# Performance work log

Measured on AMD Instinct MI355X. Metric: run time of the kernel, lower is better.

## Reference

```python
import jax, jax.numpy as jnp
import numpy as np

T, B, H = 1024, 16, 1024
S = 2048


def setup_inputs() -> dict:
    key = jax.random.key(0)
    k1, k2, k3, k4 = jax.random.split(key, 4)
    output = jax.random.normal(k1, (T, B, H), dtype=jnp.float32)
    memory = jax.random.normal(k2, (S, B, H), dtype=jnp.float32)
    attn_mask = jnp.zeros((B, T, S), dtype=jnp.bool_)  # True = masked
    # linear_out: Linear(2H -> H); torch weight layout [out, in]
    W = jax.random.normal(k3, (H, 2 * H), dtype=jnp.float32) * (1.0 / np.sqrt(2 * H))
    b = jax.random.normal(k4, (H,), dtype=jnp.float32) * 0.01
    return {"output": output, "memory": memory, "attn_mask": attn_mask, "W": W, "b": b}


def reference(output, memory, attn_mask, W, b):
    # scores: (B, T, S) = output^T @ memory (unscaled dot product)
    attn = jnp.einsum('tbh,sbh->bts', output, memory)
    attn = jnp.where(attn_mask, -jnp.inf, attn)
    attn = jax.nn.softmax(attn, axis=2)
    # context: (T, B, H)
    context = jnp.einsum('bts,sbh->tbh', attn, memory)
    combined = jnp.concatenate([context, output], axis=2)  # (T, B, 2H)
    out = jnp.tanh(jnp.einsum('tbd,hd->tbh', combined, W) + b)
    return (out, attn)
```

## Files before the change

kernel.cpp:

```cpp
#include <hip/hip_runtime.h>
#include <hip/hip_bf16.h>
#include <math.h>

#define Tn 1024
#define Bn 16
#define Hn 1024
#define Sn 2048

typedef __attribute__((ext_vector_type(8))) short bf16x8;
typedef __attribute__((ext_vector_type(8))) unsigned short u16x8;
typedef __attribute__((ext_vector_type(4))) float f32x4;

__device__ __forceinline__ unsigned short f2bf(float x) {
  unsigned u = __float_as_uint(x);
  u += 0x7fffu + ((u >> 16) & 1u);
  return (unsigned short)(u >> 16);
}
__device__ __forceinline__ float bf2f(unsigned short h) {
  return __uint_as_float(((unsigned)h) << 16);
}

__device__ __forceinline__ void gload16(const void* g, void* l) {
  __builtin_amdgcn_global_load_lds((const __attribute__((address_space(1))) void*)g,
                                   (__attribute__((address_space(3))) void*)l, 16, 0, 0);
}

__device__ __forceinline__ int xcd_swz(int bid, int nwg) {
  return (bid & 7) * (nwg >> 3) + (bid >> 3);
}

__device__ __forceinline__ f32x4 mfma16(bf16x8 a, bf16x8 b, f32x4 c) {
  return __builtin_amdgcn_mfma_f32_16x16x32_bf16(a, b, c, 0, 0, 0);
}


__global__ __launch_bounds__(256) void k_split_plane(const float* __restrict__ src,
                                                     unsigned short* __restrict__ hiP,
                                                     unsigned short* __restrict__ loP,
                                                     int rows) {
  const int i = blockIdx.x * 256 + threadIdx.x;
  const int h8 = i & (Hn / 8 - 1);
  const int rem = i >> 7;
  const int b = rem & (Bn - 1);
  const int r = rem >> 4;
  const float4 a = *(const float4*)(src + (size_t)i * 8);
  const float4 c = *(const float4*)(src + (size_t)i * 8 + 4);
  const float v[8] = {a.x, a.y, a.z, a.w, c.x, c.y, c.z, c.w};
  u16x8 hv, lv;
#pragma unroll
  for (int j = 0; j < 8; ++j) {
    const unsigned short h = f2bf(v[j]);
    hv[j] = h;
    lv[j] = f2bf(v[j] - bf2f(h));
  }
  const size_t dst = ((size_t)b * rows + r) * Hn + h8 * 8;
  *(u16x8*)(hiP + dst) = hv;
  *(u16x8*)(loP + dst) = lv;
}

__global__ __launch_bounds__(256) void k_cvt8(const float* __restrict__ src,
                                              unsigned short* __restrict__ dst, int n8) {
  const int i = blockIdx.x * 256 + threadIdx.x;
  if (i >= n8) return;
  const float4 a = *(const float4*)(src + (size_t)i * 8);
  const float4 c = *(const float4*)(src + (size_t)i * 8 + 4);
  u16x8 u;
  u[0] = f2bf(a.x); u[1] = f2bf(a.y); u[2] = f2bf(a.z); u[3] = f2bf(a.w);
  u[4] = f2bf(c.x); u[5] = f2bf(c.y); u[6] = f2bf(c.z); u[7] = f2bf(c.w);
  *(u16x8*)(dst + (size_t)i * 8) = u;
}

__global__ __launch_bounds__(256) void k_trH(const unsigned short* __restrict__ memH,
                                             unsigned short* __restrict__ memT) {
  __shared__ unsigned short L[64 * 72];
  const int t = threadIdx.x;
  const int h0 = blockIdx.x * 64, s0 = blockIdx.y * 64, b = blockIdx.z;
#pragma unroll
  for (int p = 0; p < 2; ++p) {
    const int fid = p * 256 + t;
    const int s_l = fid >> 3;
    const int c = fid & 7;
    const u16x8 v = *(const u16x8*)(memH + ((size_t)b * Sn + s0 + s_l) * Hn + h0 + c * 8);
#pragma unroll
    for (int e = 0; e < 8; ++e) L[(c * 8 + e) * 72 + s_l] = v[e];
  }
  __syncthreads();
#pragma unroll
  for (int p = 0; p < 2; ++p) {
    const int cid = p * 256 + t;
    const int h_l = cid >> 3;
    const int c = cid & 7;
    const u16x8 vv = *(const u16x8*)&L[h_l * 72 + c * 8];
    *(u16x8*)(memT + ((size_t)b * Hn + h0 + h_l) * Sn + s0 + c * 8) = vv;
  }
}


__device__ __forceinline__ void stage256x64(const unsigned short* __restrict__ g, size_t ldr,
                                            unsigned short* __restrict__ lds, int tid) {
#pragma unroll
  for (int r = 0; r < 4; ++r) {
    const int row = r * 64 + (tid >> 3);
    const int cb = (tid & 7) * 16;
    const int cs = cb ^ ((row & 7) << 4);
    gload16((const char*)g + (size_t)row * ldr * 2 + cs, (char*)lds + r * 8192 + tid * 16);
  }
}

__device__ __forceinline__ void stage256x32(const unsigned short* __restrict__ g, size_t ldr,
                                            unsigned short* __restrict__ lds, int tid) {
#pragma unroll
  for (int r = 0; r < 2; ++r) {
    const int row = r * 128 + (tid >> 2);
    const int cb = (tid & 3) * 16;
    const int cs = cb ^ ((row & 8) << 2);
    gload16((const char*)g + (size_t)row * ldr * 2 + cs, (char*)lds + r * 8192 + tid * 16);
  }
}


__global__ __launch_bounds__(512, 1) void k_scores(const unsigned short* __restrict__ oH,
                                                   const unsigned short* __restrict__ oL,
                                                   const unsigned short* __restrict__ mH,
                                                   const unsigned short* __restrict__ mL,
                                                   float* __restrict__ attn) {
  __shared__ unsigned short AsH[2][256 * 32], AsL[2][256 * 32];
  __shared__ unsigned short BsH[2][256 * 32], BsL[2][256 * 32];
  const int tid = threadIdx.x, lane = tid & 63, wv = tid >> 6;
  const int wr = wv >> 2, wc = wv & 3;
  const int swz = xcd_swz(blockIdx.x, 512);
  const int bs = (swz & 7) * 256;
  const int bt = ((swz >> 3) & 3) * 256;
  const int b = swz >> 5;
  const f32x4 fz = {0.f, 0.f, 0.f, 0.f};
  f32x4 acc[8][4];
#pragma unroll
  for (int i = 0; i < 8; ++i)
#pragma unroll
    for (int j = 0; j < 4; ++j) acc[i][j] = fz;

  const unsigned short* AgH = oH + ((size_t)b * Tn + bt) * Hn;
  const unsigned short* AgL = oL + ((size_t)b * Tn + bt) * Hn;
  const unsigned short* BgH = mH + ((size_t)b * Sn + bs) * Hn;
  const unsigned short* BgL = mL + ((size_t)b * Sn + bs) * Hn;
  const int r16 = lane & 15, khB = (lane >> 4) * 16;
  const int NK = Hn / 32;

  stage256x32(AgH, Hn, AsH[0], tid);
  stage256x32(AgL, Hn, AsL[0], tid);
  stage256x32(BgH, Hn, BsH[0], tid);
  stage256x32(BgL, Hn, BsL[0], tid);

  for (int t = 0; t < NK; ++t) {
    const int cur = t & 1;
    asm volatile("s_waitcnt vmcnt(0)" ::: "memory");
    __builtin_amdgcn_s_barrier();

    const bool st = (t + 1) < NK;
    const int k1 = (t + 1) * 32;
    const char* ABh = (const char*)AsH[cur];
    const char* ABl = (const char*)AsL[cur];
    const char* BBh = (const char*)BsH[cur];
    const char* BBl = (const char*)BsL[cur];

    if (st) {
      stage256x32(AgH + k1, Hn, AsH[cur ^ 1], tid);
      stage256x32(AgL + k1, Hn, AsL[cur ^ 1], tid);
    }

    bf16x8 bh[2][2], bl[2][2];
#pragma unroll
    for (int nq = 0; nq < 2; ++nq)
#pragma unroll
      for (int fj = 0; fj < 2; ++fj) {
        const int rb = wc * 64 + nq * 32 + fj * 16 + r16;
        const int off = rb * 64 + (khB ^ ((rb & 8) << 2));
        bh[nq][fj] = *(const bf16x8*)(BBh + off);
        bl[nq][fj] = *(const bf16x8*)(BBl + off);
      }
    bf16x8 ah0[4], al0[4];
#pragma unroll
    for (int fi = 0; fi < 4; ++fi) {
      const int ra = wr * 128 + fi * 16 + r16;
      const int off = ra * 64 + (khB ^ ((ra & 8) << 2));
      ah0[fi] = *(const bf16x8*)(ABh + off);
      al0[fi] = *(const bf16x8*)(ABl + off);
    }
    __builtin_amdgcn_s_setprio(1);
#pragma unroll
    for (int nq = 0; nq < 2; ++nq)
#pragma unroll
      for (int fj = 0; fj < 2; ++fj)
#pragma unroll
        for (int fi = 0; fi < 4; ++fi) {
          f32x4& a = acc[fi][nq * 2 + fj];
          a = mfma16(ah0[fi], bh[nq][fj], a);
          a = mfma16(ah0[fi], bl[nq][fj], a);
          a = mfma16(al0[fi], bh[nq][fj], a);
        }
    __builtin_amdgcn_s_setprio(0);

    if (st) {
      stage256x32(BgH + k1, Hn, BsH[cur ^ 1], tid);
      stage256x32(BgL + k1, Hn, BsL[cur ^ 1], tid);
    }
    bf16x8 ah1[4], al1[4];
#pragma unroll
    for (int fi = 0; fi < 4; ++fi) {
      const int ra = wr * 128 + 64 + fi * 16 + r16;
      const int off = ra * 64 + (khB ^ ((ra & 8) << 2));
      ah1[fi] = *(const bf16x8*)(ABh + off);
      al1[fi] = *(const bf16x8*)(ABl + off);
    }
    __builtin_amdgcn_s_setprio(1);
#pragma unroll
    for (int nq = 0; nq < 2; ++nq)
#pragma unroll
      for (int fj = 0; fj < 2; ++fj)
#pragma unroll
        for (int fi = 0; fi < 4; ++fi) {
          f32x4& a = acc[4 + fi][nq * 2 + fj];
          a = mfma16(ah1[fi], bh[nq][fj], a);
          a = mfma16(ah1[fi], bl[nq][fj], a);
          a = mfma16(al1[fi], bh[nq][fj], a);
        }
    __builtin_amdgcn_s_setprio(0);
  }

  const int rq = (lane >> 4) * 4;
  float* obase = attn + (size_t)b * Tn * Sn;
#pragma unroll
  for (int i = 0; i < 8; ++i) {
    const int m_off = wr * 128 + (i >> 2) * 64 + (i & 3) * 16;
#pragma unroll
    for (int q = 0; q < 4; ++q) {
      const int t = bt + m_off + rq + q;
#pragma unroll
      for (int j = 0; j < 4; ++j) {
        const int s = bs + wc * 64 + (j >> 1) * 32 + (j & 1) * 16 + r16;
        obase[(size_t)t * Sn + s] = acc[i][j][q];
      }
    }
  }
}


__global__ __launch_bounds__(256) void k_softmax(float* __restrict__ attn,
                                                 const unsigned char* __restrict__ mask,
                                                 unsigned short* __restrict__ attnbf) {
  const int row = blockIdx.x;
  float* p = attn + (size_t)row * Sn;
  const unsigned char* mrow = mask + (size_t)row * Sn;
  const int tid = threadIdx.x;
  const int lane = tid & 63;
  const int wv = tid >> 6;
  const float4 a = *(const float4*)(p + tid * 8);
  const float4 c = *(const float4*)(p + tid * 8 + 4);
  const unsigned long long mv = *(const unsigned long long*)(mrow + tid * 8);
  float x[8] = {a.x, a.y, a.z, a.w, c.x, c.y, c.z, c.w};
#pragma unroll
  for (int j = 0; j < 8; ++j)
    if ((mv >> (8 * j)) & 0xffull) x[j] = -INFINITY;
  float mx = x[0];
#pragma unroll
  for (int j = 1; j < 8; ++j) mx = fmaxf(mx, x[j]);
#pragma unroll
  for (int off = 32; off; off >>= 1) mx = fmaxf(mx, __shfl_xor(mx, off, 64));
  __shared__ float redmax[4], redsum[4];
  if (lane == 0) redmax[wv] = mx;
  __syncthreads();
  mx = fmaxf(fmaxf(redmax[0], redmax[1]), fmaxf(redmax[2], redmax[3]));
  float e[8];
  float s = 0.f;
#pragma unroll
  for (int j = 0; j < 8; ++j) {
    e[j] = __expf(x[j] - mx);
    s += e[j];
  }
#pragma unroll
  for (int off = 32; off; off >>= 1) s += __shfl_xor(s, off, 64);
  if (lane == 0) redsum[wv] = s;
  __syncthreads();
  s = redsum[0] + redsum[1] + redsum[2] + redsum[3];
  const float inv = 1.0f / s;
  float o[8];
#pragma unroll
  for (int j = 0; j < 8; ++j) o[j] = e[j] * inv;
  float4 o0 = {o[0], o[1], o[2], o[3]};
  float4 o1 = {o[4], o[5], o[6], o[7]};
  *(float4*)(p + tid * 8) = o0;
  *(float4*)(p + tid * 8 + 4) = o1;
  u16x8 ub;
#pragma unroll
  for (int j = 0; j < 8; ++j) ub[j] = f2bf(o[j]);
  *(u16x8*)(attnbf + (size_t)row * Sn + tid * 8) = ub;
}


__global__ __launch_bounds__(512, 2) void k_context(const unsigned short* __restrict__ attnbf,
                                                    const unsigned short* __restrict__ memT,
                                                    unsigned short* __restrict__ ctxB) {
  __shared__ unsigned short As[2][256 * 64], Bs[2][256 * 64];
  const int tid = threadIdx.x, lane = tid & 63, wv = tid >> 6;
  const int wr = wv >> 2, wc = wv & 3;
  const int swz = xcd_swz(blockIdx.x, 256);
  const int bh = (swz & 3) * 256;
  const int bt = ((swz >> 2) & 3) * 256;
  const int b = swz >> 4;
  const f32x4 fz = {0.f, 0.f, 0.f, 0.f};
  f32x4 acc[8][4];
#pragma unroll
  for (int i = 0; i < 8; ++i)
#pragma unroll
    for (int j = 0; j < 4; ++j) acc[i][j] = fz;

  const unsigned short* Ag = attnbf + ((size_t)b * Tn + bt) * Sn;
  const unsigned short* Bg = memT + ((size_t)b * Hn + bh) * Sn;
  const int r16 = lane & 15, khB = (lane >> 4) * 16;
  const int NK = Sn / 64;

  stage256x64(Ag, Sn, As[0], tid);
  stage256x64(Bg, Sn, Bs[0], tid);

  for (int t = 0; t < NK; ++t) {
    const int cur = t & 1;
    if (t + 1 < NK) {
      const int k0 = (t + 1) * 64;
      stage256x64(Ag + k0, Sn, As[cur ^ 1], tid);
      stage256x64(Bg + k0, Sn, Bs[cur ^ 1], tid);
      asm volatile("s_waitcnt vmcnt(8)" ::: "memory");
    } else {
      asm volatile("s_waitcnt vmcnt(0)" ::: "memory");
    }
    __builtin_amdgcn_s_barrier();

    const char* Ab = (const char*)As[cur];
    const char* Bb = (const char*)Bs[cur];
    bf16x8 bb[2][2][2];
#pragma unroll
    for (int nq = 0; nq < 2; ++nq)
#pragma unroll
      for (int fj = 0; fj < 2; ++fj) {
        const int rb = wc * 64 + nq * 32 + fj * 16 + r16;
#pragma unroll
        for (int ks = 0; ks < 2; ++ks) {
          const int cb = ks * 64 + khB;
          bb[nq][fj][ks] = *(const bf16x8*)(Bb + rb * 128 + (cb ^ ((rb & 7) << 4)));
        }
      }
#pragma unroll
    for (int mq = 0; mq < 2; ++mq) {
      bf16x8 aa[4][2];
#pragma unroll
      for (int fi = 0; fi < 4; ++fi) {
        const int ra = wr * 128 + mq * 64 + fi * 16 + r16;
#pragma unroll
        for (int ks = 0; ks < 2; ++ks) {
          const int cb = ks * 64 + khB;
          aa[fi][ks] = *(const bf16x8*)(Ab + ra * 128 + (cb ^ ((ra & 7) << 4)));
        }
      }
      __builtin_amdgcn_s_setprio(1);
#pragma unroll
      for (int nq = 0; nq < 2; ++nq)
#pragma unroll
        for (int fj = 0; fj < 2; ++fj)
#pragma unroll
          for (int fi = 0; fi < 4; ++fi)
#pragma unroll
            for (int ks = 0; ks < 2; ++ks) {
              f32x4& a = acc[mq * 4 + fi][nq * 2 + fj];
              a = mfma16(aa[fi][ks], bb[nq][fj][ks], a);
            }
      __builtin_amdgcn_s_setprio(0);
    }
    __builtin_amdgcn_s_barrier();
  }
  const int rq = (lane >> 4) * 4;
#pragma unroll
  for (int i = 0; i < 8; ++i) {
    const int m_off = wr * 128 + (i >> 2) * 64 + (i & 3) * 16;
#pragma unroll
    for (int q = 0; q < 4; ++q) {
      const int t = bt + m_off + rq + q;
#pragma unroll
      for (int j = 0; j < 4; ++j) {
        const int h = bh + wc * 64 + (j >> 1) * 32 + (j & 1) * 16 + r16;
        ctxB[((size_t)b * Tn + t) * Hn + h] = f2bf(acc[i][j][q]);
      }
    }
  }
}


__global__ __launch_bounds__(512, 2) void k_final(const unsigned short* __restrict__ ctxB,
                                                  const unsigned short* __restrict__ outpH,
                                                  const unsigned short* __restrict__ Wbf,
                                                  const float* __restrict__ bias,
                                                  float* __restrict__ out) {
  __shared__ unsigned short As[2][256 * 64], Bs[2][256 * 64];
  const int tid = threadIdx.x, lane = tid & 63, wv = tid >> 6;
  const int wr = wv >> 2, wc = wv & 3;
  const int swz = xcd_swz(blockIdx.x, 256);
  const int bh = (swz & 3) * 256;
  const int bm = (swz >> 2) * 256;
  const f32x4 fz = {0.f, 0.f, 0.f, 0.f};
  f32x4 acc[8][4];
#pragma unroll
  for (int i = 0; i < 8; ++i)
#pragma unroll
    for (int j = 0; j < 4; ++j) acc[i][j] = fz;

  const int r16 = lane & 15, khB = (lane >> 4) * 16;
  const int NK = (2 * Hn) / 64;
  auto Asrc = [&](int tt) -> const unsigned short* {
    return (tt < 16) ? (ctxB + (size_t)bm * Hn + tt * 64)
                     : (outpH + (size_t)bm * Hn + (tt - 16) * 64);
  };
  const unsigned short* Bg = Wbf + (size_t)bh * (2 * Hn);

  stage256x64(Asrc(0), Hn, As[0], tid);
  stage256x64(Bg, 2 * Hn, Bs[0], tid);

  for (int t = 0; t < NK; ++t) {
    const int cur = t & 1;
    if (t + 1 < NK) {
      stage256x64(Asrc(t + 1), Hn, As[cur ^ 1], tid);
      stage256x64(Bg + (t + 1) * 64, 2 * Hn, Bs[cur ^ 1], tid);
      asm volatile("s_waitcnt vmcnt(8)" ::: "memory");
    } else {
      asm volatile("s_waitcnt vmcnt(0)" ::: "memory");
    }
    __builtin_amdgcn_s_barrier();

    const char* Ab = (const char*)As[cur];
    const char* Bb = (const char*)Bs[cur];
    bf16x8 bb[2][2][2];
#pragma unroll
    for (int nq = 0; nq < 2; ++nq)
#pragma unroll
      for (int fj = 0; fj < 2; ++fj) {
        const int rb = wc * 64 + nq * 32 + fj * 16 + r16;
#pragma unroll
        for (int ks = 0; ks < 2; ++ks) {
          const int cb = ks * 64 + khB;
          bb[nq][fj][ks] = *(const bf16x8*)(Bb + rb * 128 + (cb ^ ((rb & 7) << 4)));
        }
      }
#pragma unroll
    for (int mq = 0; mq < 2; ++mq) {
      bf16x8 aa[4][2];
#pragma unroll
      for (int fi = 0; fi < 4; ++fi) {
        const int ra = wr * 128 + mq * 64 + fi * 16 + r16;
#pragma unroll
        for (int ks = 0; ks < 2; ++ks) {
          const int cb = ks * 64 + khB;
          aa[fi][ks] = *(const bf16x8*)(Ab + ra * 128 + (cb ^ ((ra & 7) << 4)));
        }
      }
      __builtin_amdgcn_s_setprio(1);
#pragma unroll
      for (int nq = 0; nq < 2; ++nq)
#pragma unroll
        for (int fj = 0; fj < 2; ++fj)
#pragma unroll
          for (int fi = 0; fi < 4; ++fi)
#pragma unroll
            for (int ks = 0; ks < 2; ++ks) {
              f32x4& a = acc[mq * 4 + fi][nq * 2 + fj];
              a = mfma16(aa[fi][ks], bb[nq][fj][ks], a);
            }
      __builtin_amdgcn_s_setprio(0);
    }
    __builtin_amdgcn_s_barrier();
  }
  const int rq = (lane >> 4) * 4;
#pragma unroll
  for (int i = 0; i < 8; ++i) {
    const int m_off = wr * 128 + (i >> 2) * 64 + (i & 3) * 16;
#pragma unroll
    for (int q = 0; q < 4; ++q) {
      const int r = bm + m_off + rq + q;
      const int b = r >> 10, t = r & (Tn - 1);
#pragma unroll
      for (int j = 0; j < 4; ++j) {
        const int h = bh + wc * 64 + (j >> 1) * 32 + (j & 1) * 16 + r16;
        out[((size_t)t * Bn + b) * Hn + h] = tanhf(acc[i][j][q] + bias[h]);
      }
    }
  }
}

extern "C" void kernel_launch(void* const* d_in, const int* in_sizes, int n_in,
                              void* d_out, int out_size, void* d_ws, size_t ws_size,
                              hipStream_t stream) {
  const float* outp = (const float*)d_in[0];
  const float* mem = (const float*)d_in[1];
  const unsigned char* mask = (const unsigned char*)d_in[2];
  const float* W = (const float*)d_in[3];
  const float* bias = (const float*)d_in[4];
  float* out = (float*)d_out;
  float* attn = out + (size_t)Tn * Bn * Hn;

  char* w = (char*)d_ws;
  unsigned short* memH  = (unsigned short*)(w);
  unsigned short* memL  = (unsigned short*)(w + ((size_t)64 << 20));
  unsigned short* outpH = (unsigned short*)(w + ((size_t)128 << 20));
  unsigned short* outpL = (unsigned short*)(w + ((size_t)160 << 20));
  unsigned short* Wbf   = (unsigned short*)(w + ((size_t)192 << 20));
  unsigned short* memT   = memL;
  unsigned short* attnbf = memH;
  unsigned short* ctxB   = outpL;

  k_split_plane<<<dim3((Tn * Bn * Hn / 8) / 256), 256, 0, stream>>>(outp, outpH, outpL, Tn);
  k_split_plane<<<dim3((Sn * Bn * Hn / 8) / 256), 256, 0, stream>>>(mem, memH, memL, Sn);
  k_cvt8<<<dim3((Hn * 2 * Hn / 8) / 256), 256, 0, stream>>>(W, Wbf, Hn * 2 * Hn / 8);

  k_scores<<<dim3(512), 512, 0, stream>>>(outpH, outpL, memH, memL, attn);
  k_trH<<<dim3(Hn / 64, Sn / 64, Bn), 256, 0, stream>>>(memH, memT);
  k_softmax<<<dim3(Bn * Tn), 256, 0, stream>>>(attn, mask, attnbf);
  k_context<<<dim3(256), 512, 0, stream>>>(attnbf, memT, ctxB);
  k_final<<<dim3(256), 512, 0, stream>>>(ctxB, outpH, Wbf, bias, out);
}
```

Baseline: 516.0 us.

## Fuse memory split with transpose and restage GEMM prefetch within compute

Merges the hi/lo split of memory and the transpose into one kernel, which writes memH, memL and memT from a single fp32 read. This removes a separate transpose pass that re-read memH, and memT moves to its own workspace region. The context and final GEMM loops now issue next-tile A and B loads between the two MFMA half-blocks, with a full vmcnt(0) wait plus one barrier per iteration instead of two. The LDS transpose write also gets a rotated element order to spread bank conflicts. Risks: the added global write of memT in the split kernel, and less latency hiding from waiting on all loads.

```diff
diff --git a/kernel.cpp b/kernel.cpp
--- a/kernel.cpp
+++ b/kernel.cpp
@@ -70,19 +70,37 @@
   *(u16x8*)(dst + (size_t)i * 8) = u;
 }
 
-__global__ __launch_bounds__(256) void k_trH(const unsigned short* __restrict__ memH,
-                                             unsigned short* __restrict__ memT) {
+__global__ __launch_bounds__(256) void k_split_mem3(const float* __restrict__ mem,
+                                                    unsigned short* __restrict__ memH,
+                                                    unsigned short* __restrict__ memL,
+                                                    unsigned short* __restrict__ memT) {
   __shared__ unsigned short L[64 * 72];
   const int t = threadIdx.x;
   const int h0 = blockIdx.x * 64, s0 = blockIdx.y * 64, b = blockIdx.z;
 #pragma unroll
   for (int p = 0; p < 2; ++p) {
-    const int fid = p * 256 + t;
-    const int s_l = fid >> 3;
-    const int c = fid & 7;
-    const u16x8 v = *(const u16x8*)(memH + ((size_t)b * Sn + s0 + s_l) * Hn + h0 + c * 8);
-#pragma unroll
-    for (int e = 0; e < 8; ++e) L[(c * 8 + e) * 72 + s_l] = v[e];
+    const int id = p * 256 + t;
+    const int row = id >> 3;
+    const int c8 = id & 7;
+    const float* src = mem + ((size_t)(s0 + row) * Bn + b) * Hn + h0 + c8 * 8;
+    const float4 a = *(const float4*)src;
+    const float4 c = *(const float4*)(src + 4);
+    const float v[8] = {a.x, a.y, a.z, a.w, c.x, c.y, c.z, c.w};
+    u16x8 hv, lv;
+#pragma unroll
+    for (int j = 0; j < 8; ++j) {
+      const unsigned short h = f2bf(v[j]);
+      hv[j] = h;
+      lv[j] = f2bf(v[j] - bf2f(h));
+    }
+    const size_t dst = ((size_t)b * Sn + s0 + row) * Hn + h0 + c8 * 8;
+    *(u16x8*)(memH + dst) = hv;
+    *(u16x8*)(memL + dst) = lv;
+#pragma unroll
+    for (int e0 = 0; e0 < 8; ++e0) {
+      const int e = (e0 + (t >> 3)) & 7;
+      L[(c8 * 8 + e) * 72 + row] = hv[e];
+    }
   }
   __syncthreads();
 #pragma unroll
@@ -324,18 +342,16 @@
 
   for (int t = 0; t < NK; ++t) {
     const int cur = t & 1;
-    if (t + 1 < NK) {
-      const int k0 = (t + 1) * 64;
-      stage256x64(Ag + k0, Sn, As[cur ^ 1], tid);
-      stage256x64(Bg + k0, Sn, Bs[cur ^ 1], tid);
-      asm volatile("s_waitcnt vmcnt(8)" ::: "memory");
-    } else {
-      asm volatile("s_waitcnt vmcnt(0)" ::: "memory");
-    }
+    asm volatile("s_waitcnt vmcnt(0)" ::: "memory");
     __builtin_amdgcn_s_barrier();
 
+    const bool st = (t + 1) < NK;
+    const int k1 = (t + 1) * 64;
     const char* Ab = (const char*)As[cur];
     const char* Bb = (const char*)Bs[cur];
+
+    if (st) stage256x64(Ag + k1, Sn, As[cur ^ 1], tid);
+
     bf16x8 bb[2][2][2];
 #pragma unroll
     for (int nq = 0; nq < 2; ++nq)
@@ -348,33 +364,51 @@
           bb[nq][fj][ks] = *(const bf16x8*)(Bb + rb * 128 + (cb ^ ((rb & 7) << 4)));
         }
       }
-#pragma unroll
-    for (int mq = 0; mq < 2; ++mq) {
-      bf16x8 aa[4][2];
-#pragma unroll
-      for (int fi = 0; fi < 4; ++fi) {
-        const int ra = wr * 128 + mq * 64 + fi * 16 + r16;
-#pragma unroll
-        for (int ks = 0; ks < 2; ++ks) {
-          const int cb = ks * 64 + khB;
-          aa[fi][ks] = *(const bf16x8*)(Ab + ra * 128 + (cb ^ ((ra & 7) << 4)));
-        }
-      }
-      __builtin_amdgcn_s_setprio(1);
-#pragma unroll
-      for (int nq = 0; nq < 2; ++nq)
-#pragma unroll
-        for (int fj = 0; fj < 2; ++fj)
-#pragma unroll
-          for (int fi = 0; fi < 4; ++fi)
-#pragma unroll
-            for (int ks = 0; ks < 2; ++ks) {
-              f32x4& a = acc[mq * 4 + fi][nq * 2 + fj];
-              a = mfma16(aa[fi][ks], bb[nq][fj][ks], a);
-            }
-      __builtin_amdgcn_s_setprio(0);
-    }
-    __builtin_amdgcn_s_barrier();
+    bf16x8 aa0[4][2];
+#pragma unroll
+    for (int fi = 0; fi < 4; ++fi) {
+      const int ra = wr * 128 + fi * 16 + r16;
+#pragma unroll
+      for (int ks = 0; ks < 2; ++ks) {
+        const int cb = ks * 64 + khB;
+        aa0[fi][ks] = *(const bf16x8*)(Ab + ra * 128 + (cb ^ ((ra & 7) << 4)));
+      }
+    }
+    __builtin_amdgcn_s_setprio(1);
+#pragma unroll
+    for (int nq = 0; nq < 2; ++nq)
+#pragma unroll
+      for (int fj = 0; fj < 2; ++fj)
+#pragma unroll
+        for (int fi = 0; fi < 4; ++fi)
+#pragma unroll
+          for (int ks = 0; ks < 2; ++ks)
+            acc[fi][nq * 2 + fj] = mfma16(aa0[fi][ks], bb[nq][fj][ks], acc[fi][nq * 2 + fj]);
+    __builtin_amdgcn_s_setprio(0);
+
+    if (st) stage256x64(Bg + k1, Sn, Bs[cur ^ 1], tid);
+
+    bf16x8 aa1[4][2];
+#pragma unroll
+    for (int fi = 0; fi < 4; ++fi) {
+      const int ra = wr * 128 + 64 + fi * 16 + r16;
+#pragma unroll
+      for (int ks = 0; ks < 2; ++ks) {
+        const int cb = ks * 64 + khB;
+        aa1[fi][ks] = *(const bf16x8*)(Ab + ra * 128 + (cb ^ ((ra & 7) << 4)));
+      }
+    }
+    __builtin_amdgcn_s_setprio(1);
+#pragma unroll
+    for (int nq = 0; nq < 2; ++nq)
+#pragma unroll
+      for (int fj = 0; fj < 2; ++fj)
+#pragma unroll
+        for (int fi = 0; fi < 4; ++fi)
+#pragma unroll
+          for (int ks = 0; ks < 2; ++ks)
+            acc[4 + fi][nq * 2 + fj] = mfma16(aa1[fi][ks], bb[nq][fj][ks], acc[4 + fi][nq * 2 + fj]);
+    __builtin_amdgcn_s_setprio(0);
   }
   const int rq = (lane >> 4) * 4;
 #pragma unroll
@@ -424,17 +458,15 @@
 
   for (int t = 0; t < NK; ++t) {
     const int cur = t & 1;
-    if (t + 1 < NK) {
-      stage256x64(Asrc(t + 1), Hn, As[cur ^ 1], tid);
-      stage256x64(Bg + (t + 1) * 64, 2 * Hn, Bs[cur ^ 1], tid);
-      asm volatile("s_waitcnt vmcnt(8)" ::: "memory");
-    } else {
-      asm volatile("s_waitcnt vmcnt(0)" ::: "memory");
-    }
+    asm volatile("s_waitcnt vmcnt(0)" ::: "memory");
     __builtin_amdgcn_s_barrier();
 
+    const bool st = (t + 1) < NK;
     const char* Ab = (const char*)As[cur];
     const char* Bb = (const char*)Bs[cur];
+
+    if (st) stage256x64(Asrc(t + 1), Hn, As[cur ^ 1], tid);
+
     bf16x8 bb[2][2][2];
 #pragma unroll
     for (int nq = 0; nq < 2; ++nq)
@@ -447,33 +479,51 @@
           bb[nq][fj][ks] = *(const bf16x8*)(Bb + rb * 128 + (cb ^ ((rb & 7) << 4)));
         }
       }
-#pragma unroll
-    for (int mq = 0; mq < 2; ++mq) {
-      bf16x8 aa[4][2];
-#pragma unroll
-      for (int fi = 0; fi < 4; ++fi) {
-        const int ra = wr * 128 + mq * 64 + fi * 16 + r16;
-#pragma unroll
-        for (int ks = 0; ks < 2; ++ks) {
-          const int cb = ks * 64 + khB;
-          aa[fi][ks] = *(const bf16x8*)(Ab + ra * 128 + (cb ^ ((ra & 7) << 4)));
-        }
-      }
-      __builtin_amdgcn_s_setprio(1);
-#pragma unroll
-      for (int nq = 0; nq < 2; ++nq)
-#pragma unroll
-        for (int fj = 0; fj < 2; ++fj)
-#pragma unroll
-          for (int fi = 0; fi < 4; ++fi)
-#pragma unroll
-            for (int ks = 0; ks < 2; ++ks) {
-              f32x4& a = acc[mq * 4 + fi][nq * 2 + fj];
-              a = mfma16(aa[fi][ks], bb[nq][fj][ks], a);
-            }
-      __builtin_amdgcn_s_setprio(0);
-    }
-    __builtin_amdgcn_s_barrier();
+    bf16x8 aa0[4][2];
+#pragma unroll
+    for (int fi = 0; fi < 4; ++fi) {
+      const int ra = wr * 128 + fi * 16 + r16;
+#pragma unroll
+      for (int ks = 0; ks < 2; ++ks) {
+        const int cb = ks * 64 + khB;
+        aa0[fi][ks] = *(const bf16x8*)(Ab + ra * 128 + (cb ^ ((ra & 7) << 4)));
+      }
+    }
+    __builtin_amdgcn_s_setprio(1);
+#pragma unroll
+    for (int nq = 0; nq < 2; ++nq)
+#pragma unroll
+      for (int fj = 0; fj < 2; ++fj)
+#pragma unroll
+        for (int fi = 0; fi < 4; ++fi)
+#pragma unroll
+          for (int ks = 0; ks < 2; ++ks)
+            acc[fi][nq * 2 + fj] = mfma16(aa0[fi][ks], bb[nq][fj][ks], acc[fi][nq * 2 + fj]);
+    __builtin_amdgcn_s_setprio(0);
+
+    if (st) stage256x64(Bg + (t + 1) * 64, 2 * Hn, Bs[cur ^ 1], tid);
+
+    bf16x8 aa1[4][2];
+#pragma unroll
+    for (int fi = 0; fi < 4; ++fi) {
+      const int ra = wr * 128 + 64 + fi * 16 + r16;
+#pragma unroll
+      for (int ks = 0; ks < 2; ++ks) {
+        const int cb = ks * 64 + khB;
+        aa1[fi][ks] = *(const bf16x8*)(Ab + ra * 128 + (cb ^ ((ra & 7) << 4)));
+      }
+    }
+    __builtin_amdgcn_s_setprio(1);
+#pragma unroll
+    for (int nq = 0; nq < 2; ++nq)
+#pragma unroll
+      for (int fj = 0; fj < 2; ++fj)
+#pragma unroll
+        for (int fi = 0; fi < 4; ++fi)
+#pragma unroll
+          for (int ks = 0; ks < 2; ++ks)
+            acc[4 + fi][nq * 2 + fj] = mfma16(aa1[fi][ks], bb[nq][fj][ks], acc[4 + fi][nq * 2 + fj]);
+    __builtin_amdgcn_s_setprio(0);
   }
   const int rq = (lane >> 4) * 4;
 #pragma unroll
@@ -509,16 +559,15 @@
   unsigned short* outpH = (unsigned short*)(w + ((size_t)128 << 20));
   unsigned short* outpL = (unsigned short*)(w + ((size_t)160 << 20));
   unsigned short* Wbf   = (unsigned short*)(w + ((size_t)192 << 20));
-  unsigned short* memT   = memL;
+  unsigned short* memT  = (unsigned short*)(w + ((size_t)196 << 20));
   unsigned short* attnbf = memH;
   unsigned short* ctxB   = outpL;
 
   k_split_plane<<<dim3((Tn * Bn * Hn / 8) / 256), 256, 0, stream>>>(outp, outpH, outpL, Tn);
-  k_split_plane<<<dim3((Sn * Bn * Hn / 8) / 256), 256, 0, stream>>>(mem, memH, memL, Sn);
+  k_split_mem3<<<dim3(Hn / 64, Sn / 64, Bn), 256, 0, stream>>>(mem, memH, memL, memT);
   k_cvt8<<<dim3((Hn * 2 * Hn / 8) / 256), 256, 0, stream>>>(W, Wbf, Hn * 2 * Hn / 8);
 
   k_scores<<<dim3(512), 512, 0, stream>>>(outpH, outpL, memH, memL, attn);
-  k_trH<<<dim3(Hn / 64, Sn / 64, Bn), 256, 0, stream>>>(memH, memT);
   k_softmax<<<dim3(Bn * Tn), 256, 0, stream>>>(attn, mask, attnbf);
   k_context<<<dim3(256), 512, 0, stream>>>(attnbf, memT, ctxB);
   k_final<<<dim3(256), 512, 0, stream>>>(ctxB, outpH, Wbf, bias, out);
```

After: 517.1 us. About the same (+0.2%).
